# Optimization experiments

Measured on AMD Instinct MI355X. Metric: run time of the kernel, lower is better.

The kernel has to match this reference:

```python
import jax, jax.numpy as jnp
import numpy as np

N = 100000  # nodes
E = 1600000  # edges


def gcn_layer(x, src, dst, W, b, n):
    # GCNConv with normalize=True: add self-loops, symmetric deg normalization,
    # linear transform, scatter-add aggregate, add bias, then ReLU (applied by caller).
    loop = jnp.arange(n, dtype=src.dtype)
    s = jnp.concatenate([src, loop])
    d = jnp.concatenate([dst, loop])
    w = jnp.ones(s.shape[0], x.dtype)
    deg = jax.ops.segment_sum(w, d, num_segments=n)
    dis = jnp.where(deg > 0, jax.lax.rsqrt(deg), 0.0)
    norm = dis[s] * w * dis[d]            # [E+N]
    h = x @ W                              # [N, out]
    msg = h[s] * norm[:, None]             # [E+N, out] gather + scale
    out = jax.ops.segment_sum(msg, d, num_segments=n) + b
    return out


def setup_inputs() -> dict:
    key = jax.random.key(0)
    ks = jax.random.split(key, 8)
    d = 128
    sc = 0.05
    return {
        "x": jax.random.normal(ks[0], (N, d), jnp.float32),
        "edge_index": jax.random.randint(ks[1], (2, E), 0, N, jnp.int32),
        "W1": jax.random.normal(ks[2], (d, d), jnp.float32) * sc,
        "b1": jnp.zeros((d,), jnp.float32),
        "W2": jax.random.normal(ks[3], (d, d), jnp.float32) * sc,
        "b2": jnp.zeros((d,), jnp.float32),
        "W3": jax.random.normal(ks[4], (d, d), jnp.float32) * sc,
        "b3": jnp.zeros((d,), jnp.float32),
        "Wm1": jax.random.normal(ks[5], (d, d), jnp.float32) * sc,
        "bm1": jnp.zeros((d,), jnp.float32),
        "Wm2": jax.random.normal(ks[6], (d, 40), jnp.float32) * sc,
        "bm2": jnp.zeros((40,), jnp.float32),
    }


def reference(x, edge_index, W1, b1, W2, b2, W3, b3, Wm1, bm1, Wm2, bm2):
    src, dst = edge_index[0], edge_index[1]
    n = x.shape[0]
    h = x
    for W, b in ((W1, b1), (W2, b2), (W3, b3)):
        h = jax.nn.relu(gcn_layer(h, src, dst, W, b, n))  # emb_normlize=False
    emb = h  # concate=False -> last layer output
    # MLP head: Linear -> ELU -> (dropout p=0, eval) -> Linear -> softmax
    m = jax.nn.elu(emb @ Wm1 + bm1)
    logits = m @ Wm2 + bm2
    probs = jax.nn.softmax(logits, axis=-1)
    return (logits, probs, emb)
```

## Files before the change

### kernel.cpp

```cpp
#include <hip/hip_runtime.h>
#include <math.h>

#define D 128
#define BINW 256
#define MAXBIN 400
#define ACHUNK 4096
#define BCAP 6144

typedef __attribute__((ext_vector_type(8))) short short8;
typedef __attribute__((ext_vector_type(4))) float floatx4;
typedef __attribute__((ext_vector_type(8))) _Float16 half8;


__global__ __launch_bounds__(256) void k_zero(int* __restrict__ p, int n) {
  int i = blockIdx.x * 256 + threadIdx.x;
  if (i < n) p[i] = 0;
}

__global__ __launch_bounds__(256) void k_binhist(const int* __restrict__ dst,
                                                 int* __restrict__ gbinc,
                                                 int E, int nbin) {
  __shared__ int h[MAXBIN];
  for (int i = threadIdx.x; i < nbin; i += 256) h[i] = 0;
  __syncthreads();
  int stride = gridDim.x * 256;
  for (int e = blockIdx.x * 256 + (int)threadIdx.x; e < E; e += stride)
    atomicAdd(&h[dst[e] >> 8], 1);
  __syncthreads();
  for (int i = threadIdx.x; i < nbin; i += 256)
    if (h[i]) atomicAdd(&gbinc[i], h[i]);
}

__global__ __launch_bounds__(256) void k_binscan(const int* __restrict__ gbinc,
                                                 int* __restrict__ binoff,
                                                 int* __restrict__ gbincur, int nbin) {
  __shared__ int hv[512];
  __shared__ int sd[256];
  int tid = threadIdx.x;
  for (int i = tid; i < 512; i += 256) hv[i] = (i < nbin) ? gbinc[i] : 0;
  __syncthreads();
  int a = hv[2 * tid], b = hv[2 * tid + 1];
  int s = a + b;
  sd[tid] = s;
  __syncthreads();
  for (int off = 1; off < 256; off <<= 1) {
    int t = (tid >= off) ? sd[tid - off] : 0;
    __syncthreads();
    sd[tid] += t;
    __syncthreads();
  }
  int excl = sd[tid] - s;
  if (2 * tid < nbin)     { binoff[2 * tid] = excl;         gbincur[2 * tid] = excl; }
  if (2 * tid + 1 < nbin) { binoff[2 * tid + 1] = excl + a; gbincur[2 * tid + 1] = excl + a; }
  if (tid == 255) binoff[nbin] = sd[255];
}

__global__ __launch_bounds__(256) void k_passA(const int* __restrict__ src,
                                               const int* __restrict__ dst,
                                               int* __restrict__ gbincur,
                                               unsigned* __restrict__ staging,
                                               int E, int nbin) {
  __shared__ int hist[MAXBIN];
  __shared__ int lstart[MAXBIN];
  __shared__ int lcur[MAXBIN];
  __shared__ int runbase[MAXBIN];
  __shared__ int sd[256];
  __shared__ unsigned sbuf[ACHUNK];

  int tid = threadIdx.x;
  int e0 = blockIdx.x * ACHUNK;
  int e1 = e0 + ACHUNK < E ? e0 + ACHUNK : E;

  for (int i = tid; i < nbin; i += 256) hist[i] = 0;
  __syncthreads();
  for (int e = e0 + tid; e < e1; e += 256) atomicAdd(&hist[dst[e] >> 8], 1);
  __syncthreads();

  int a = (2 * tid < nbin) ? hist[2 * tid] : 0;
  int b = (2 * tid + 1 < nbin) ? hist[2 * tid + 1] : 0;
  int s = a + b;
  sd[tid] = s;
  __syncthreads();
  for (int off = 1; off < 256; off <<= 1) {
    int t = (tid >= off) ? sd[tid - off] : 0;
    __syncthreads();
    sd[tid] += t;
    __syncthreads();
  }
  int excl = sd[tid] - s;
  if (2 * tid < nbin) lstart[2 * tid] = excl;
  if (2 * tid + 1 < nbin) lstart[2 * tid + 1] = excl + a;
  __syncthreads();

  for (int bx = tid; bx < nbin; bx += 256) {
    int cb = hist[bx];
    runbase[bx] = cb ? atomicAdd(&gbincur[bx], cb) : 0;
    lcur[bx] = lstart[bx];
  }
  __syncthreads();

  for (int e = e0 + tid; e < e1; e += 256) {
    int dd = dst[e];
    int bb = dd >> 8;
    int p = atomicAdd(&lcur[bb], 1);
    sbuf[p] = ((unsigned)src[e] << 8) | (unsigned)(dd & 255);
  }
  __syncthreads();

  int wv = tid >> 6, ln = tid & 63;
  for (int bx = wv; bx < nbin; bx += 4) {
    int cb = hist[bx], ls = lstart[bx], rb = runbase[bx];
    for (int i = ln; i < cb; i += 64) staging[rb + i] = sbuf[ls + i];
  }
}

__global__ __launch_bounds__(256) void k_nodehist(const unsigned* __restrict__ staging,
                                                  const int* __restrict__ binoff,
                                                  int* __restrict__ counts, int N) {
  __shared__ int cnt[BINW];
  int b = blockIdx.x;
  cnt[threadIdx.x] = 0;
  __syncthreads();
  int s = binoff[b], e = binoff[b + 1];
  for (int i = s + (int)threadIdx.x; i < e; i += 256)
    atomicAdd(&cnt[staging[i] & 255], 1);
  __syncthreads();
  int node = b * BINW + (int)threadIdx.x;
  if (node < N) counts[node] = cnt[threadIdx.x];
}

__global__ __launch_bounds__(256) void k_scan1(const int* __restrict__ in,
                                               int* __restrict__ out,
                                               int* __restrict__ bsum, int n) {
  __shared__ int sd[256];
  int tid = threadIdx.x;
  int base = blockIdx.x * 1024 + tid * 4;
  int v0 = 0, v1 = 0, v2 = 0, v3 = 0;
  if (base + 3 < n) {
    int4 t = *(const int4*)(in + base);
    v0 = t.x; v1 = t.y; v2 = t.z; v3 = t.w;
  } else {
    if (base     < n) v0 = in[base];
    if (base + 1 < n) v1 = in[base + 1];
    if (base + 2 < n) v2 = in[base + 2];
    if (base + 3 < n) v3 = in[base + 3];
  }
  int s = v0 + v1 + v2 + v3;
  sd[tid] = s;
  __syncthreads();
  for (int off = 1; off < 256; off <<= 1) {
    int t = (tid >= off) ? sd[tid - off] : 0;
    __syncthreads();
    sd[tid] += t;
    __syncthreads();
  }
  int incl = sd[tid];
  int excl = incl - s;
  if (tid == 255) bsum[blockIdx.x] = incl;
  int r = excl;
  if (base     < n) out[base]     = r; r += v0;
  if (base + 1 < n) out[base + 1] = r; r += v1;
  if (base + 2 < n) out[base + 2] = r; r += v2;
  if (base + 3 < n) out[base + 3] = r;
}

__global__ __launch_bounds__(256) void k_scan2(int* __restrict__ bsum, int nb) {
  __shared__ int sd[256];
  int tid = threadIdx.x;
  int v = (tid < nb) ? bsum[tid] : 0;
  sd[tid] = v;
  __syncthreads();
  for (int off = 1; off < 256; off <<= 1) {
    int t = (tid >= off) ? sd[tid - off] : 0;
    __syncthreads();
    sd[tid] += t;
    __syncthreads();
  }
  int excl = sd[tid] - v;
  if (tid < nb) bsum[tid] = excl;
}

__global__ __launch_bounds__(256) void k_finish(int* __restrict__ rowptr,
                                                float* __restrict__ dis,
                                                const int* __restrict__ counts,
                                                const int* __restrict__ bsum, int n) {
  int i = blockIdx.x * 256 + threadIdx.x;
  if (i < n) {
    int r = rowptr[i] + bsum[i >> 10];
    rowptr[i] = r;
    dis[i] = rsqrtf((float)(counts[i] + 1));
  }
}

__global__ __launch_bounds__(256) void k_passB2(const unsigned* __restrict__ staging,
                                                const int* __restrict__ binoff,
                                                const int* __restrict__ rowptr,
                                                const float* __restrict__ dis,
                                                int2* __restrict__ cpack, int N) {
  __shared__ int lcnt[BINW];
  __shared__ int2 obuf[BCAP];
  int b = blockIdx.x, tid = threadIdx.x;
  int node0 = b * BINW;
  int s = binoff[b], e = binoff[b + 1];
  int len = e - s;
  int base = rowptr[node0];
  int node = node0 + tid;
  lcnt[tid] = (node < N) ? (rowptr[node] - base) : 0;
  __syncthreads();
  if (len <= BCAP) {
    for (int i = s + tid; i < e; i += 256) {
      unsigned pk = staging[i];
      int sn = (int)(pk >> 8), dl = (int)(pk & 255u);
      float nw = dis[sn] * dis[node0 + dl];
      int p = atomicAdd(&lcnt[dl], 1);
      obuf[p] = make_int2(sn, __float_as_int(nw));
    }
    __syncthreads();
    for (int i = tid; i < len; i += 256) cpack[base + i] = obuf[i];
  } else {
    for (int i = s + tid; i < e; i += 256) {
      unsigned pk = staging[i];
      int sn = (int)(pk >> 8), dl = (int)(pk & 255u);
      float nw = dis[sn] * dis[node0 + dl];
      int p = atomicAdd(&lcnt[dl], 1);
      cpack[base + p] = make_int2(sn, __float_as_int(nw));
    }
  }
}


__device__ __forceinline__ short f2bf(float v) {
  unsigned u = __float_as_uint(v);
  unsigned r = (u + 0x7FFFu + ((u >> 16) & 1u)) >> 16;
  return (short)r;
}
__device__ __forceinline__ float bf2f(short s) {
  return __uint_as_float(((unsigned)(unsigned short)s) << 16);
}

__global__ __launch_bounds__(256) void k_prep(const float* __restrict__ W1,
                                              const float* __restrict__ W2,
                                              const float* __restrict__ W3,
                                              const float* __restrict__ Wm1,
                                              const float* __restrict__ Wm2,
                                              short* __restrict__ wsplit,
                                              short* __restrict__ w2hi,
                                              short* __restrict__ w2lo) {
  int idx = blockIdx.x * 256 + threadIdx.x;
  if (idx < 65536) {
    int w = idx >> 14;
    int rem = idx & 16383;
    int c = rem >> 7, k = rem & 127;
    const float* Ws = (w == 0) ? W1 : (w == 1) ? W2 : (w == 2) ? W3 : Wm1;
    float v = Ws[k * D + c];
    short hi = f2bf(v);
    short lo = f2bf(v - bf2f(hi));
    wsplit[(size_t)w * 32768 + rem] = hi;
    wsplit[(size_t)w * 32768 + 16384 + rem] = lo;
  } else if (idx < 65536 + 6144) {
    int i2 = idx - 65536;
    int c = i2 >> 7, k = i2 & 127;
    float v = (c < 40) ? Wm2[k * 40 + c] : 0.f;
    short hi = f2bf(v);
    short lo = f2bf(v - bf2f(hi));
    w2hi[i2] = hi;
    w2lo[i2] = lo;
  }
}


__device__ __forceinline__ float elu1(float x) {
  return x > 0.f ? x : (expf(x) - 1.f);
}

__global__ __launch_bounds__(256, 2) void k_gemm(const float* __restrict__ Xf,
                                                 const _Float16* __restrict__ Xh,
                                                 const short* __restrict__ Whi,
                                                 const short* __restrict__ Wlo,
                                                 const float* __restrict__ bias,
                                                 _Float16* __restrict__ Yh,
                                                 int n, int act, int amode) {
  __shared__ short wthi[128 * 72];
  __shared__ short wtlo[128 * 72];

  int tid = threadIdx.x;
  int wave = tid >> 6, lane = tid & 63;
  int q = lane >> 4, r = lane & 15;

  long rowbase = (long)blockIdx.x * 128 + wave * 32;
  long row0 = rowbase + r;
  long row1 = rowbase + 16 + r;
  long rc0 = row0 < n ? row0 : (n - 1);
  long rc1 = row1 < n ? row1 : (n - 1);

  floatx4 acc[2][8];
#pragma unroll
  for (int rt = 0; rt < 2; rt++)
#pragma unroll
    for (int ct = 0; ct < 8; ct++) acc[rt][ct] = (floatx4){0.f, 0.f, 0.f, 0.f};

  for (int h = 0; h < 2; h++) {
    __syncthreads();
#pragma unroll
    for (int i = 0; i < 4; i++) {
      int cs = i * 256 + tid;
      int c = cs >> 3, o = (cs & 7) * 8;
      *(short8*)&wthi[c * 72 + o] = *(const short8*)&Whi[c * D + h * 64 + o];
      *(short8*)&wtlo[c * 72 + o] = *(const short8*)&Wlo[c * D + h * 64 + o];
    }
    __syncthreads();

#pragma unroll
    for (int ks2 = 0; ks2 < 2; ks2++) {
      int ksg = h * 2 + ks2;
      int kk0 = ks2 * 32;
      short8 ahi0, alo0, ahi1, alo1;
      if (amode == 2) {
        half8 a0 = *(const half8*)(Xh + rc0 * D + ksg * 32 + q * 8);
        half8 a1 = *(const half8*)(Xh + rc1 * D + ksg * 32 + q * 8);
#pragma unroll
        for (int j = 0; j < 8; j++) {
          float v = (float)a0[j];
          short hi = f2bf(v);
          ahi0[j] = hi; alo0[j] = f2bf(v - bf2f(hi));
          v = (float)a1[j];
          hi = f2bf(v);
          ahi1[j] = hi; alo1[j] = f2bf(v - bf2f(hi));
        }
      } else {
        const floatx4* x0 = (const floatx4*)(Xf + rc0 * D);
        const floatx4* x1 = (const floatx4*)(Xf + rc1 * D);
        int xi = ksg * 8 + q * 2;
        floatx4 a0 = x0[xi], a0b = x0[xi + 1];
        floatx4 a1 = x1[xi], a1b = x1[xi + 1];
#pragma unroll
        for (int j = 0; j < 4; j++) {
          float v = a0[j];  short hi = f2bf(v);
          ahi0[j] = hi; alo0[j] = f2bf(v - bf2f(hi));
          v = a0b[j]; hi = f2bf(v);
          ahi0[4 + j] = hi; alo0[4 + j] = f2bf(v - bf2f(hi));
          v = a1[j];  hi = f2bf(v);
          ahi1[j] = hi; alo1[j] = f2bf(v - bf2f(hi));
          v = a1b[j]; hi = f2bf(v);
          ahi1[4 + j] = hi; alo1[4 + j] = f2bf(v - bf2f(hi));
        }
      }
#pragma unroll
      for (int ct = 0; ct < 8; ct++) {
        int c = ct * 16 + r;
        short8 bh = *(const short8*)&wthi[c * 72 + kk0 + q * 8];
        short8 bl = *(const short8*)&wtlo[c * 72 + kk0 + q * 8];
        acc[0][ct] = __builtin_amdgcn_mfma_f32_16x16x32_bf16(ahi0, bh, acc[0][ct], 0, 0, 0);
        acc[0][ct] = __builtin_amdgcn_mfma_f32_16x16x32_bf16(alo0, bh, acc[0][ct], 0, 0, 0);
        acc[0][ct] = __builtin_amdgcn_mfma_f32_16x16x32_bf16(ahi0, bl, acc[0][ct], 0, 0, 0);
        acc[1][ct] = __builtin_amdgcn_mfma_f32_16x16x32_bf16(ahi1, bh, acc[1][ct], 0, 0, 0);
        acc[1][ct] = __builtin_amdgcn_mfma_f32_16x16x32_bf16(alo1, bh, acc[1][ct], 0, 0, 0);
        acc[1][ct] = __builtin_amdgcn_mfma_f32_16x16x32_bf16(ahi1, bl, acc[1][ct], 0, 0, 0);
      }
    }
  }

#pragma unroll
  for (int rt = 0; rt < 2; rt++) {
#pragma unroll
    for (int i = 0; i < 4; i++) {
      long row = rowbase + rt * 16 + q * 4 + i;
      if (row < n) {
#pragma unroll
        for (int ct = 0; ct < 8; ct++) {
          int col = ct * 16 + r;
          float v = acc[rt][ct][i];
          if (bias) v += bias[col];
          if (act == 1) v = elu1(v);
          Yh[row * D + col] = (_Float16)v;
        }
      }
    }
  }
}


__global__ __launch_bounds__(256) void k_agg(const _Float16* __restrict__ T,
                                             const int* __restrict__ rowptr,
                                             const int* __restrict__ counts,
                                             const int2* __restrict__ cpack,
                                             const float* __restrict__ dis,
                                             const float* __restrict__ bias,
                                             _Float16* __restrict__ Yh,
                                             float* __restrict__ Yf, int n) {
  int tid = threadIdx.x;
  int wave = tid >> 6;
  int lane = tid & 63;
  int g = lane >> 4;
  int r16 = lane & 15;
  int node = blockIdx.x * 16 + wave * 4 + g;
  bool actv = node < n;
  int nodec = actv ? node : 0;

  const half8* T8 = (const half8*)T;

  int s = actv ? rowptr[nodec] : 0;
  int c = actv ? counts[nodec] : 0;
  float dv = actv ? dis[nodec] : 0.f;
  float dv2 = dv * dv;

  half8 t = T8[(size_t)nodec * 16 + r16];
  float acc[8];
#pragma unroll
  for (int k = 0; k < 8; k++) acc[k] = (float)t[k] * dv2;

  int j = 0;
  for (; j + 3 < c; j += 4) {
    int2 m0 = cpack[s + j];
    int2 m1 = cpack[s + j + 1];
    int2 m2 = cpack[s + j + 2];
    int2 m3 = cpack[s + j + 3];
    half8 v0 = T8[(size_t)m0.x * 16 + r16];
    half8 v1 = T8[(size_t)m1.x * 16 + r16];
    half8 v2 = T8[(size_t)m2.x * 16 + r16];
    half8 v3 = T8[(size_t)m3.x * 16 + r16];
    float n0 = __int_as_float(m0.y), n1 = __int_as_float(m1.y);
    float n2 = __int_as_float(m2.y), n3 = __int_as_float(m3.y);
#pragma unroll
    for (int k = 0; k < 8; k++) {
      acc[k] += (float)v0[k] * n0;
      acc[k] += (float)v1[k] * n1;
      acc[k] += (float)v2[k] * n2;
      acc[k] += (float)v3[k] * n3;
    }
  }
  for (; j < c; ++j) {
    int2 m = cpack[s + j];
    half8 v = T8[(size_t)m.x * 16 + r16];
    float nw = __int_as_float(m.y);
#pragma unroll
    for (int k = 0; k < 8; k++) acc[k] += (float)v[k] * nw;
  }

  if (actv) {
    const floatx4* b4 = (const floatx4*)(bias + r16 * 8);
    floatx4 bb0 = b4[0], bb1 = b4[1];
    half8 oh;
    float of[8];
#pragma unroll
    for (int k = 0; k < 8; k++) {
      float bv = (k < 4) ? bb0[k] : bb1[k - 4];
      float o = fmaxf(acc[k] + bv, 0.f);
      of[k] = o;
      oh[k] = (_Float16)o;
    }
    *(half8*)&Yh[(size_t)node * D + r16 * 8] = oh;
    if (Yf) {
      floatx4 o0 = {of[0], of[1], of[2], of[3]};
      floatx4 o1 = {of[4], of[5], of[6], of[7]};
      floatx4* yp = (floatx4*)(Yf + (size_t)node * D + r16 * 8);
      yp[0] = o0;
      yp[1] = o1;
    }
  }
}


__global__ __launch_bounds__(256) void k_head(const _Float16* __restrict__ M,
                                              const short* __restrict__ Whi,
                                              const short* __restrict__ Wlo,
                                              const float* __restrict__ b,
                                              float* __restrict__ logits,
                                              float* __restrict__ probs, int n) {
  int tid = threadIdx.x;
  int wave = tid >> 6, lane = tid & 63;
  int q = lane >> 4, r = lane & 15;

  long rowbase = (long)blockIdx.x * 128 + wave * 32;
  long row0 = rowbase + r;
  long row1 = rowbase + 16 + r;
  long rc0 = row0 < n ? row0 : (n - 1);
  long rc1 = row1 < n ? row1 : (n - 1);

  floatx4 acc[2][3];
#pragma unroll
  for (int rt = 0; rt < 2; rt++)
#pragma unroll
    for (int ct = 0; ct < 3; ct++) acc[rt][ct] = (floatx4){0.f, 0.f, 0.f, 0.f};

#pragma unroll
  for (int ks = 0; ks < 4; ks++) {
    half8 a0 = *(const half8*)(M + rc0 * D + ks * 32 + q * 8);
    half8 a1 = *(const half8*)(M + rc1 * D + ks * 32 + q * 8);
    short8 ahi0, alo0, ahi1, alo1;
#pragma unroll
    for (int j = 0; j < 8; j++) {
      float v = (float)a0[j];
      short hi = f2bf(v);
      ahi0[j] = hi; alo0[j] = f2bf(v - bf2f(hi));
      v = (float)a1[j];
      hi = f2bf(v);
      ahi1[j] = hi; alo1[j] = f2bf(v - bf2f(hi));
    }
#pragma unroll
    for (int ct = 0; ct < 3; ct++) {
      int c = ct * 16 + r;
      short8 bh = *(const short8*)&Whi[c * D + ks * 32 + q * 8];
      short8 bl = *(const short8*)&Wlo[c * D + ks * 32 + q * 8];
      acc[0][ct] = __builtin_amdgcn_mfma_f32_16x16x32_bf16(ahi0, bh, acc[0][ct], 0, 0, 0);
      acc[0][ct] = __builtin_amdgcn_mfma_f32_16x16x32_bf16(alo0, bh, acc[0][ct], 0, 0, 0);
      acc[0][ct] = __builtin_amdgcn_mfma_f32_16x16x32_bf16(ahi0, bl, acc[0][ct], 0, 0, 0);
      acc[1][ct] = __builtin_amdgcn_mfma_f32_16x16x32_bf16(ahi1, bh, acc[1][ct], 0, 0, 0);
      acc[1][ct] = __builtin_amdgcn_mfma_f32_16x16x32_bf16(alo1, bh, acc[1][ct], 0, 0, 0);
      acc[1][ct] = __builtin_amdgcn_mfma_f32_16x16x32_bf16(ahi1, bl, acc[1][ct], 0, 0, 0);
    }
  }

  float bb0 = b[r];
  float bb1 = b[16 + r];
  float bb2 = (r < 8) ? b[32 + r] : 0.f;

#pragma unroll
  for (int rt = 0; rt < 2; rt++) {
#pragma unroll
    for (int i = 0; i < 4; i++) {
      long row = rowbase + rt * 16 + q * 4 + i;
      float v0 = acc[rt][0][i] + bb0;
      float v1 = acc[rt][1][i] + bb1;
      float v2 = (r < 8) ? (acc[rt][2][i] + bb2) : -INFINITY;
      float mx = fmaxf(fmaxf(v0, v1), v2);
      mx = fmaxf(mx, __shfl_xor(mx, 1));
      mx = fmaxf(mx, __shfl_xor(mx, 2));
      mx = fmaxf(mx, __shfl_xor(mx, 4));
      mx = fmaxf(mx, __shfl_xor(mx, 8));
      float e0 = expf(v0 - mx);
      float e1 = expf(v1 - mx);
      float e2 = (r < 8) ? expf(v2 - mx) : 0.f;
      float sm = e0 + e1 + e2;
      sm += __shfl_xor(sm, 1);
      sm += __shfl_xor(sm, 2);
      sm += __shfl_xor(sm, 4);
      sm += __shfl_xor(sm, 8);
      float inv = 1.f / sm;
      if (row < n) {
        float* lp = logits + row * 40;
        float* pp = probs + row * 40;
        lp[r] = v0;      pp[r] = e0 * inv;
        lp[16 + r] = v1; pp[16 + r] = e1 * inv;
        if (r < 8) { lp[32 + r] = v2; pp[32 + r] = e2 * inv; }
      }
    }
  }
}


extern "C" void kernel_launch(void* const* d_in, const int* in_sizes, int n_in,
                              void* d_out, int out_size, void* d_ws, size_t ws_size,
                              hipStream_t stream) {
  const float* x   = (const float*)d_in[0];
  const int*   ei  = (const int*)d_in[1];
  const float* W1  = (const float*)d_in[2];
  const float* b1  = (const float*)d_in[3];
  const float* W2  = (const float*)d_in[4];
  const float* b2  = (const float*)d_in[5];
  const float* W3  = (const float*)d_in[6];
  const float* b3  = (const float*)d_in[7];
  const float* Wm1 = (const float*)d_in[8];
  const float* bm1 = (const float*)d_in[9];
  const float* Wm2 = (const float*)d_in[10];
  const float* bm2 = (const float*)d_in[11];

  int N = in_sizes[0] / D;
  int E = in_sizes[1] / 2;
  const int* srcp = ei;
  const int* dstp = ei + E;
  int NBIN = (N + BINW - 1) / BINW;

  char* w = (char*)d_ws;
  auto alloc = [&](size_t bytes) -> char* {
    char* p = w;
    w += (bytes + 255) & ~(size_t)255;
    return p;
  };
  int*   counts = (int*)alloc((size_t)N * 4);
  int*   rowptr = (int*)alloc((size_t)N * 4);
  float* dis    = (float*)alloc((size_t)N * 4);
  int*   bsum   = (int*)alloc(1024);
  int*   gbinc  = (int*)alloc(MAXBIN * 4);
  int*   binoff = (int*)alloc((MAXBIN + 1) * 4);
  int*   gbincur= (int*)alloc(MAXBIN * 4);
  short* wsplit = (short*)alloc(4 * 32768 * 2);
  short* w2hi   = (short*)alloc(6144 * 2);
  short* w2lo   = (short*)alloc(6144 * 2);
  int2*  cpack  = (int2*)alloc((size_t)E * 8);
  _Float16* tmp_h  = (_Float16*)alloc((size_t)N * D * 2);
  _Float16* hbuf_h = (_Float16*)alloc((size_t)N * D * 2);
  unsigned* staging = (unsigned*)tmp_h;

  float* logits = (float*)d_out;
  float* probs  = logits + (size_t)N * 40;
  float* emb    = probs + (size_t)N * 40;

  k_prep<<<(65536 + 6144 + 255) / 256, 256, 0, stream>>>(W1, W2, W3, Wm1, Wm2,
                                                         wsplit, w2hi, w2lo);
  k_zero<<<(NBIN + 255) / 256, 256, 0, stream>>>(gbinc, NBIN);
  k_binhist<<<256, 256, 0, stream>>>(dstp, gbinc, E, NBIN);
  k_binscan<<<1, 256, 0, stream>>>(gbinc, binoff, gbincur, NBIN);
  k_passA<<<(E + ACHUNK - 1) / ACHUNK, 256, 0, stream>>>(srcp, dstp, gbincur,
                                                         staging, E, NBIN);
  k_nodehist<<<NBIN, 256, 0, stream>>>(staging, binoff, counts, N);
  int nb = (N + 1023) / 1024;
  k_scan1<<<nb, 256, 0, stream>>>(counts, rowptr, bsum, N);
  k_scan2<<<1, 256, 0, stream>>>(bsum, nb);
  k_finish<<<(N + 255) / 256, 256, 0, stream>>>(rowptr, dis, counts, bsum, N);
  k_passB2<<<NBIN, 256, 0, stream>>>(staging, binoff, rowptr, dis, cpack, N);

  int gblocks = (N + 127) / 128;
  int ablocks = (N + 15) / 16;
  const short* Whi1 = wsplit;
  const short* Wlo1 = wsplit + 16384;
  const short* Whi2 = wsplit + 32768;
  const short* Wlo2 = wsplit + 32768 + 16384;
  const short* Whi3 = wsplit + 2 * 32768;
  const short* Wlo3 = wsplit + 2 * 32768 + 16384;
  const short* Whm1 = wsplit + 3 * 32768;
  const short* Wlm1 = wsplit + 3 * 32768 + 16384;

  k_gemm<<<gblocks, 256, 0, stream>>>(x, nullptr, Whi1, Wlo1, nullptr,
                                      tmp_h, N, 0, 0);
  k_agg<<<ablocks, 256, 0, stream>>>(tmp_h, rowptr, counts, cpack, dis, b1,
                                     hbuf_h, nullptr, N);
  k_gemm<<<gblocks, 256, 0, stream>>>(nullptr, hbuf_h, Whi2, Wlo2, nullptr,
                                      tmp_h, N, 0, 2);
  k_agg<<<ablocks, 256, 0, stream>>>(tmp_h, rowptr, counts, cpack, dis, b2,
                                     hbuf_h, nullptr, N);
  k_gemm<<<gblocks, 256, 0, stream>>>(nullptr, hbuf_h, Whi3, Wlo3, nullptr,
                                      tmp_h, N, 0, 2);
  k_agg<<<ablocks, 256, 0, stream>>>(tmp_h, rowptr, counts, cpack, dis, b3,
                                     hbuf_h, emb, N);
  k_gemm<<<gblocks, 256, 0, stream>>>(nullptr, hbuf_h, Whm1, Wlm1, bm1,
                                      tmp_h, N, 1, 2);
  k_head<<<gblocks, 256, 0, stream>>>(tmp_h, w2hi, w2lo, bm2,
                                      logits, probs, N);
}
```

Before: 582.6 us.

## Switch split-precision GEMMs from bf16 to fp16 MFMA and unroll aggregation

Measured after the change: 630.3 us. 1.08x slower.

```diff
diff --git a/kernel.cpp b/kernel.cpp
--- a/kernel.cpp
+++ b/kernel.cpp
@@ -7,7 +7,6 @@
 #define ACHUNK 4096
 #define BCAP 6144
 
-typedef __attribute__((ext_vector_type(8))) short short8;
 typedef __attribute__((ext_vector_type(4))) float floatx4;
 typedef __attribute__((ext_vector_type(8))) _Float16 half8;
 
@@ -229,23 +228,14 @@
 }
 
 
-__device__ __forceinline__ short f2bf(float v) {
-  unsigned u = __float_as_uint(v);
-  unsigned r = (u + 0x7FFFu + ((u >> 16) & 1u)) >> 16;
-  return (short)r;
-}
-__device__ __forceinline__ float bf2f(short s) {
-  return __uint_as_float(((unsigned)(unsigned short)s) << 16);
-}
-
 __global__ __launch_bounds__(256) void k_prep(const float* __restrict__ W1,
                                               const float* __restrict__ W2,
                                               const float* __restrict__ W3,
                                               const float* __restrict__ Wm1,
                                               const float* __restrict__ Wm2,
-                                              short* __restrict__ wsplit,
-                                              short* __restrict__ w2hi,
-                                              short* __restrict__ w2lo) {
+                                              _Float16* __restrict__ wsplit,
+                                              _Float16* __restrict__ w2h,
+                                              _Float16* __restrict__ w2l) {
   int idx = blockIdx.x * 256 + threadIdx.x;
   if (idx < 65536) {
     int w = idx >> 14;
@@ -253,18 +243,18 @@
     int c = rem >> 7, k = rem & 127;
     const float* Ws = (w == 0) ? W1 : (w == 1) ? W2 : (w == 2) ? W3 : Wm1;
     float v = Ws[k * D + c];
-    short hi = f2bf(v);
-    short lo = f2bf(v - bf2f(hi));
+    _Float16 hi = (_Float16)v;
+    _Float16 lo = (_Float16)(v - (float)hi);
     wsplit[(size_t)w * 32768 + rem] = hi;
     wsplit[(size_t)w * 32768 + 16384 + rem] = lo;
   } else if (idx < 65536 + 6144) {
     int i2 = idx - 65536;
     int c = i2 >> 7, k = i2 & 127;
     float v = (c < 40) ? Wm2[k * 40 + c] : 0.f;
-    short hi = f2bf(v);
-    short lo = f2bf(v - bf2f(hi));
-    w2hi[i2] = hi;
-    w2lo[i2] = lo;
+    _Float16 hi = (_Float16)v;
+    _Float16 lo = (_Float16)(v - (float)hi);
+    w2h[i2] = hi;
+    w2l[i2] = lo;
   }
 }
 
@@ -273,16 +263,13 @@
   return x > 0.f ? x : (expf(x) - 1.f);
 }
 
-__global__ __launch_bounds__(256, 2) void k_gemm(const float* __restrict__ Xf,
+__global__ __launch_bounds__(256, 4) void k_gemm(const float* __restrict__ Xf,
                                                  const _Float16* __restrict__ Xh,
-                                                 const short* __restrict__ Whi,
-                                                 const short* __restrict__ Wlo,
+                                                 const _Float16* __restrict__ Whf,
+                                                 const _Float16* __restrict__ Wlf,
                                                  const float* __restrict__ bias,
                                                  _Float16* __restrict__ Yh,
                                                  int n, int act, int amode) {
-  __shared__ short wthi[128 * 72];
-  __shared__ short wtlo[128 * 72];
-
   int tid = threadIdx.x;
   int wave = tid >> 6, lane = tid & 63;
   int q = lane >> 4, r = lane & 15;
@@ -299,63 +286,42 @@
 #pragma unroll
     for (int ct = 0; ct < 8; ct++) acc[rt][ct] = (floatx4){0.f, 0.f, 0.f, 0.f};
 
-  for (int h = 0; h < 2; h++) {
-    __syncthreads();
-#pragma unroll
-    for (int i = 0; i < 4; i++) {
-      int cs = i * 256 + tid;
-      int c = cs >> 3, o = (cs & 7) * 8;
-      *(short8*)&wthi[c * 72 + o] = *(const short8*)&Whi[c * D + h * 64 + o];
-      *(short8*)&wtlo[c * 72 + o] = *(const short8*)&Wlo[c * D + h * 64 + o];
-    }
-    __syncthreads();
-
-#pragma unroll
-    for (int ks2 = 0; ks2 < 2; ks2++) {
-      int ksg = h * 2 + ks2;
-      int kk0 = ks2 * 32;
-      short8 ahi0, alo0, ahi1, alo1;
-      if (amode == 2) {
-        half8 a0 = *(const half8*)(Xh + rc0 * D + ksg * 32 + q * 8);
-        half8 a1 = *(const half8*)(Xh + rc1 * D + ksg * 32 + q * 8);
-#pragma unroll
-        for (int j = 0; j < 8; j++) {
-          float v = (float)a0[j];
-          short hi = f2bf(v);
-          ahi0[j] = hi; alo0[j] = f2bf(v - bf2f(hi));
-          v = (float)a1[j];
-          hi = f2bf(v);
-          ahi1[j] = hi; alo1[j] = f2bf(v - bf2f(hi));
-        }
-      } else {
-        const floatx4* x0 = (const floatx4*)(Xf + rc0 * D);
-        const floatx4* x1 = (const floatx4*)(Xf + rc1 * D);
-        int xi = ksg * 8 + q * 2;
-        floatx4 a0 = x0[xi], a0b = x0[xi + 1];
-        floatx4 a1 = x1[xi], a1b = x1[xi + 1];
-#pragma unroll
-        for (int j = 0; j < 4; j++) {
-          float v = a0[j];  short hi = f2bf(v);
-          ahi0[j] = hi; alo0[j] = f2bf(v - bf2f(hi));
-          v = a0b[j]; hi = f2bf(v);
-          ahi0[4 + j] = hi; alo0[4 + j] = f2bf(v - bf2f(hi));
-          v = a1[j];  hi = f2bf(v);
-          ahi1[j] = hi; alo1[j] = f2bf(v - bf2f(hi));
-          v = a1b[j]; hi = f2bf(v);
-          ahi1[4 + j] = hi; alo1[4 + j] = f2bf(v - bf2f(hi));
-        }
+#pragma unroll
+  for (int ks = 0; ks < 4; ks++) {
+    half8 ah0, al0, ah1, al1;
+    if (amode == 2) {
+      ah0 = *(const half8*)(Xh + rc0 * D + ks * 32 + q * 8);
+      ah1 = *(const half8*)(Xh + rc1 * D + ks * 32 + q * 8);
+    } else {
+      const floatx4* x0 = (const floatx4*)(Xf + rc0 * D);
+      const floatx4* x1 = (const floatx4*)(Xf + rc1 * D);
+      int xi = ks * 8 + q * 2;
+      floatx4 a0 = x0[xi], a0b = x0[xi + 1];
+      floatx4 a1 = x1[xi], a1b = x1[xi + 1];
+#pragma unroll
+      for (int j = 0; j < 4; j++) {
+        float v = a0[j];  _Float16 h = (_Float16)v;
+        ah0[j] = h; al0[j] = (_Float16)(v - (float)h);
+        v = a0b[j]; h = (_Float16)v;
+        ah0[4 + j] = h; al0[4 + j] = (_Float16)(v - (float)h);
+        v = a1[j];  h = (_Float16)v;
+        ah1[j] = h; al1[j] = (_Float16)(v - (float)h);
+        v = a1b[j]; h = (_Float16)v;
+        ah1[4 + j] = h; al1[4 + j] = (_Float16)(v - (float)h);
       }
-#pragma unroll
-      for (int ct = 0; ct < 8; ct++) {
-        int c = ct * 16 + r;
-        short8 bh = *(const short8*)&wthi[c * 72 + kk0 + q * 8];
-        short8 bl = *(const short8*)&wtlo[c * 72 + kk0 + q * 8];
-        acc[0][ct] = __builtin_amdgcn_mfma_f32_16x16x32_bf16(ahi0, bh, acc[0][ct], 0, 0, 0);
-        acc[0][ct] = __builtin_amdgcn_mfma_f32_16x16x32_bf16(alo0, bh, acc[0][ct], 0, 0, 0);
-        acc[0][ct] = __builtin_amdgcn_mfma_f32_16x16x32_bf16(ahi0, bl, acc[0][ct], 0, 0, 0);
-        acc[1][ct] = __builtin_amdgcn_mfma_f32_16x16x32_bf16(ahi1, bh, acc[1][ct], 0, 0, 0);
-        acc[1][ct] = __builtin_amdgcn_mfma_f32_16x16x32_bf16(alo1, bh, acc[1][ct], 0, 0, 0);
-        acc[1][ct] = __builtin_amdgcn_mfma_f32_16x16x32_bf16(ahi1, bl, acc[1][ct], 0, 0, 0);
+    }
+#pragma unroll
+    for (int ct = 0; ct < 8; ct++) {
+      int c = ct * 16 + r;
+      half8 bh = *(const half8*)(Whf + c * D + ks * 32 + q * 8);
+      half8 bl = *(const half8*)(Wlf + c * D + ks * 32 + q * 8);
+      acc[0][ct] = __builtin_amdgcn_mfma_f32_16x16x32_f16(ah0, bh, acc[0][ct], 0, 0, 0);
+      acc[1][ct] = __builtin_amdgcn_mfma_f32_16x16x32_f16(ah1, bh, acc[1][ct], 0, 0, 0);
+      acc[0][ct] = __builtin_amdgcn_mfma_f32_16x16x32_f16(ah0, bl, acc[0][ct], 0, 0, 0);
+      acc[1][ct] = __builtin_amdgcn_mfma_f32_16x16x32_f16(ah1, bl, acc[1][ct], 0, 0, 0);
+      if (amode == 0) {
+        acc[0][ct] = __builtin_amdgcn_mfma_f32_16x16x32_f16(al0, bh, acc[0][ct], 0, 0, 0);
+        acc[1][ct] = __builtin_amdgcn_mfma_f32_16x16x32_f16(al1, bh, acc[1][ct], 0, 0, 0);
       }
     }
   }
@@ -410,11 +376,38 @@
   for (int k = 0; k < 8; k++) acc[k] = (float)t[k] * dv2;
 
   int j = 0;
+  for (; j + 7 < c; j += 8) {
+    int2 m0 = cpack[s + j],     m1 = cpack[s + j + 1];
+    int2 m2 = cpack[s + j + 2], m3 = cpack[s + j + 3];
+    int2 m4 = cpack[s + j + 4], m5 = cpack[s + j + 5];
+    int2 m6 = cpack[s + j + 6], m7 = cpack[s + j + 7];
+    half8 v0 = T8[(size_t)m0.x * 16 + r16];
+    half8 v1 = T8[(size_t)m1.x * 16 + r16];
+    half8 v2 = T8[(size_t)m2.x * 16 + r16];
+    half8 v3 = T8[(size_t)m3.x * 16 + r16];
+    half8 v4 = T8[(size_t)m4.x * 16 + r16];
+    half8 v5 = T8[(size_t)m5.x * 16 + r16];
+    half8 v6 = T8[(size_t)m6.x * 16 + r16];
+    half8 v7 = T8[(size_t)m7.x * 16 + r16];
+    float n0 = __int_as_float(m0.y), n1 = __int_as_float(m1.y);
+    float n2 = __int_as_float(m2.y), n3 = __int_as_float(m3.y);
+    float n4 = __int_as_float(m4.y), n5 = __int_as_float(m5.y);
+    float n6 = __int_as_float(m6.y), n7 = __int_as_float(m7.y);
+#pragma unroll
+    for (int k = 0; k < 8; k++) {
+      acc[k] += (float)v0[k] * n0;
+      acc[k] += (float)v1[k] * n1;
+      acc[k] += (float)v2[k] * n2;
+      acc[k] += (float)v3[k] * n3;
+      acc[k] += (float)v4[k] * n4;
+      acc[k] += (float)v5[k] * n5;
+      acc[k] += (float)v6[k] * n6;
+      acc[k] += (float)v7[k] * n7;
+    }
+  }
   for (; j + 3 < c; j += 4) {
-    int2 m0 = cpack[s + j];
-    int2 m1 = cpack[s + j + 1];
-    int2 m2 = cpack[s + j + 2];
-    int2 m3 = cpack[s + j + 3];
+    int2 m0 = cpack[s + j],     m1 = cpack[s + j + 1];
+    int2 m2 = cpack[s + j + 2], m3 = cpack[s + j + 3];
     half8 v0 = T8[(size_t)m0.x * 16 + r16];
     half8 v1 = T8[(size_t)m1.x * 16 + r16];
     half8 v2 = T8[(size_t)m2.x * 16 + r16];
@@ -462,8 +455,8 @@
 
 
 __global__ __launch_bounds__(256) void k_head(const _Float16* __restrict__ M,
-                                              const short* __restrict__ Whi,
-                                              const short* __restrict__ Wlo,
+                                              const _Float16* __restrict__ Whf,
+                                              const _Float16* __restrict__ Wlf,
                                               const float* __restrict__ b,
                                               float* __restrict__ logits,
                                               float* __restrict__ probs, int n) {
@@ -487,27 +480,15 @@
   for (int ks = 0; ks < 4; ks++) {
     half8 a0 = *(const half8*)(M + rc0 * D + ks * 32 + q * 8);
     half8 a1 = *(const half8*)(M + rc1 * D + ks * 32 + q * 8);
-    short8 ahi0, alo0, ahi1, alo1;
-#pragma unroll
-    for (int j = 0; j < 8; j++) {
-      float v = (float)a0[j];
-      short hi = f2bf(v);
-      ahi0[j] = hi; alo0[j] = f2bf(v - bf2f(hi));
-      v = (float)a1[j];
-      hi = f2bf(v);
-      ahi1[j] = hi; alo1[j] = f2bf(v - bf2f(hi));
-    }
 #pragma unroll
     for (int ct = 0; ct < 3; ct++) {
       int c = ct * 16 + r;
-      short8 bh = *(const short8*)&Whi[c * D + ks * 32 + q * 8];
-      short8 bl = *(const short8*)&Wlo[c * D + ks * 32 + q * 8];
-      acc[0][ct] = __builtin_amdgcn_mfma_f32_16x16x32_bf16(ahi0, bh, acc[0][ct], 0, 0, 0);
-      acc[0][ct] = __builtin_amdgcn_mfma_f32_16x16x32_bf16(alo0, bh, acc[0][ct], 0, 0, 0);
-      acc[0][ct] = __builtin_amdgcn_mfma_f32_16x16x32_bf16(ahi0, bl, acc[0][ct], 0, 0, 0);
-      acc[1][ct] = __builtin_amdgcn_mfma_f32_16x16x32_bf16(ahi1, bh, acc[1][ct], 0, 0, 0);
-      acc[1][ct] = __builtin_amdgcn_mfma_f32_16x16x32_bf16(alo1, bh, acc[1][ct], 0, 0, 0);
-      acc[1][ct] = __builtin_amdgcn_mfma_f32_16x16x32_bf16(ahi1, bl, acc[1][ct], 0, 0, 0);
+      half8 bh = *(const half8*)(Whf + c * D + ks * 32 + q * 8);
+      half8 bl = *(const half8*)(Wlf + c * D + ks * 32 + q * 8);
+      acc[0][ct] = __builtin_amdgcn_mfma_f32_16x16x32_f16(a0, bh, acc[0][ct], 0, 0, 0);
+      acc[1][ct] = __builtin_amdgcn_mfma_f32_16x16x32_f16(a1, bh, acc[1][ct], 0, 0, 0);
+      acc[0][ct] = __builtin_amdgcn_mfma_f32_16x16x32_f16(a0, bl, acc[0][ct], 0, 0, 0);
+      acc[1][ct] = __builtin_amdgcn_mfma_f32_16x16x32_f16(a1, bl, acc[1][ct], 0, 0, 0);
     }
   }
 
@@ -584,9 +565,9 @@
   int*   gbinc  = (int*)alloc(MAXBIN * 4);
   int*   binoff = (int*)alloc((MAXBIN + 1) * 4);
   int*   gbincur= (int*)alloc(MAXBIN * 4);
-  short* wsplit = (short*)alloc(4 * 32768 * 2);
-  short* w2hi   = (short*)alloc(6144 * 2);
-  short* w2lo   = (short*)alloc(6144 * 2);
+  _Float16* wsplit = (_Float16*)alloc(4 * 32768 * 2);
+  _Float16* w2h    = (_Float16*)alloc(6144 * 2);
+  _Float16* w2l    = (_Float16*)alloc(6144 * 2);
   int2*  cpack  = (int2*)alloc((size_t)E * 8);
   _Float16* tmp_h  = (_Float16*)alloc((size_t)N * D * 2);
   _Float16* hbuf_h = (_Float16*)alloc((size_t)N * D * 2);
@@ -597,7 +578,7 @@
   float* emb    = probs + (size_t)N * 40;
 
   k_prep<<<(65536 + 6144 + 255) / 256, 256, 0, stream>>>(W1, W2, W3, Wm1, Wm2,
-                                                         wsplit, w2hi, w2lo);
+                                                         wsplit, w2h, w2l);
   k_zero<<<(NBIN + 255) / 256, 256, 0, stream>>>(gbinc, NBIN);
   k_binhist<<<256, 256, 0, stream>>>(dstp, gbinc, E, NBIN);
   k_binscan<<<1, 256, 0, stream>>>(gbinc, binoff, gbincur, NBIN);
@@ -612,29 +593,29 @@
 
   int gblocks = (N + 127) / 128;
   int ablocks = (N + 15) / 16;
-  const short* Whi1 = wsplit;
-  const short* Wlo1 = wsplit + 16384;
-  const short* Whi2 = wsplit + 32768;
-  const short* Wlo2 = wsplit + 32768 + 16384;
-  const short* Whi3 = wsplit + 2 * 32768;
-  const short* Wlo3 = wsplit + 2 * 32768 + 16384;
-  const short* Whm1 = wsplit + 3 * 32768;
-  const short* Wlm1 = wsplit + 3 * 32768 + 16384;
-
-  k_gemm<<<gblocks, 256, 0, stream>>>(x, nullptr, Whi1, Wlo1, nullptr,
+  const _Float16* Whf1 = wsplit;
+  const _Float16* Wlf1 = wsplit + 16384;
+  const _Float16* Whf2 = wsplit + 32768;
+  const _Float16* Wlf2 = wsplit + 32768 + 16384;
+  const _Float16* Whf3 = wsplit + 2 * 32768;
+  const _Float16* Wlf3 = wsplit + 2 * 32768 + 16384;
+  const _Float16* Whm1 = wsplit + 3 * 32768;
+  const _Float16* Wlm1 = wsplit + 3 * 32768 + 16384;
+
+  k_gemm<<<gblocks, 256, 0, stream>>>(x, nullptr, Whf1, Wlf1, nullptr,
                                       tmp_h, N, 0, 0);
   k_agg<<<ablocks, 256, 0, stream>>>(tmp_h, rowptr, counts, cpack, dis, b1,
                                      hbuf_h, nullptr, N);
-  k_gemm<<<gblocks, 256, 0, stream>>>(nullptr, hbuf_h, Whi2, Wlo2, nullptr,
+  k_gemm<<<gblocks, 256, 0, stream>>>(nullptr, hbuf_h, Whf2, Wlf2, nullptr,
                                       tmp_h, N, 0, 2);
   k_agg<<<ablocks, 256, 0, stream>>>(tmp_h, rowptr, counts, cpack, dis, b2,
                                      hbuf_h, nullptr, N);
-  k_gemm<<<gblocks, 256, 0, stream>>>(nullptr, hbuf_h, Whi3, Wlo3, nullptr,
+  k_gemm<<<gblocks, 256, 0, stream>>>(nullptr, hbuf_h, Whf3, Wlf3, nullptr,
                                       tmp_h, N, 0, 2);
   k_agg<<<ablocks, 256, 0, stream>>>(tmp_h, rowptr, counts, cpack, dis, b3,
                                      hbuf_h, emb, N);
   k_gemm<<<gblocks, 256, 0, stream>>>(nullptr, hbuf_h, Whm1, Wlm1, bm1,
                                       tmp_h, N, 1, 2);
-  k_head<<<gblocks, 256, 0, stream>>>(tmp_h, w2hi, w2lo, bm2,
+  k_head<<<gblocks, 256, 0, stream>>>(tmp_h, w2h, w2l, bm2,
                                       logits, probs, N);
 }
```
